# Performance work log

Measured on AMD Instinct MI355X. Metric: run time of the kernel, lower is better.

Reference implementation:

```python
import jax, jax.numpy as jnp
import numpy as np

EPS = 1e-5
N_HEAD = 16


def layernorm(x, g, b):
    mu = jnp.mean(x, axis=-1, keepdims=True)
    var = jnp.mean(jnp.square(x - mu), axis=-1, keepdims=True)
    return (x - mu) * jax.lax.rsqrt(var + EPS) * g + b


def setup_inputs() -> dict:
    key = jax.random.key(0)
    ks = jax.random.split(key, 8)
    B, S, D = 4, 2048, 1024
    F = 4 * D
    s = 0.02
    return {
        "h": jax.random.normal(ks[0], (B, S, D), jnp.float32),
        "ln1_g": jnp.ones((D,), jnp.float32),
        "ln1_b": jnp.zeros((D,), jnp.float32),
        "wq": jax.random.normal(ks[1], (D, D), jnp.float32) * s,
        "bq": jnp.zeros((D,), jnp.float32),
        "wk": jax.random.normal(ks[2], (D, D), jnp.float32) * s,
        "bk": jnp.zeros((D,), jnp.float32),
        "wv": jax.random.normal(ks[3], (D, D), jnp.float32) * s,
        "bv": jnp.zeros((D,), jnp.float32),
        "wo": jax.random.normal(ks[4], (D, D), jnp.float32) * s,
        "bo": jnp.zeros((D,), jnp.float32),
        "ln2_g": jnp.ones((D,), jnp.float32),
        "ln2_b": jnp.zeros((D,), jnp.float32),
        "wfc": jax.random.normal(ks[5], (F, D), jnp.float32) * s,
        "bfc": jnp.zeros((F,), jnp.float32),
        "wproj": jax.random.normal(ks[6], (D, F), jnp.float32) * s,
        "bproj": jnp.zeros((D,), jnp.float32),
    }


def reference(h, ln1_g, ln1_b, wq, bq, wk, bk, wv, bv, wo, bo,
              ln2_g, ln2_b, wfc, bfc, wproj, bproj):
    B, S, D = h.shape
    H = N_HEAD
    Dh = D // H

    # --- attention sub-block ---
    r = h
    x = layernorm(h, ln1_g, ln1_b)
    q = (x @ wq.T + bq).reshape(B, S, H, Dh)
    k = (x @ wk.T + bk).reshape(B, S, H, Dh)
    v = (x @ wv.T + bv).reshape(B, S, H, Dh)

    scores = jnp.einsum("bqhd,bkhd->bhqk", q, k) / jnp.sqrt(jnp.float32(Dh))
    causal = jnp.tril(jnp.ones((S, S), bool))  # [S,S]
    scores = jnp.where(causal, scores, jnp.finfo(scores.dtype).min)
    probs = jax.nn.softmax(scores, axis=-1)
    o = jnp.einsum("bhqk,bkhd->bqhd", probs, v).reshape(B, S, D)
    h = r + (o @ wo.T + bo)

    # --- MLP sub-block ---
    r = h
    x = layernorm(h, ln2_g, ln2_b)
    x = jax.nn.gelu(x @ wfc.T + bfc, approximate=True)  # NewGELU (tanh)
    h = r + (x @ wproj.T + bproj)
    return h
```

## Files before the change

### kernel.cpp

```cpp
#include <hip/hip_runtime.h>
#include <hip/hip_bf16.h>
#include <stdint.h>


typedef short bf16x8 __attribute__((ext_vector_type(8)));
typedef float f32x4  __attribute__((ext_vector_type(4)));
typedef float f32x16 __attribute__((ext_vector_type(16)));
typedef short s16x4  __attribute__((ext_vector_type(4)));

__device__ __forceinline__ short f2bf(float f) {
  union { float f; uint32_t u; } a;
  a.f = f;
  uint32_t r = a.u + 0x7fffu + ((a.u >> 16) & 1u);
  return (short)(r >> 16);
}

__device__ __forceinline__ unsigned cvt_pk_bf16(float lo, float hi_) {
  unsigned r;
  asm("v_cvt_pk_bf16_f32 %0, %1, %2" : "=v"(r) : "v"(lo), "v"(hi_));
  return r;
}

__device__ __forceinline__ float ex2(float x) {
  float r;
  asm("v_exp_f32 %0, %1" : "=v"(r) : "v"(x));
  return r;
}

__device__ __forceinline__ float rcp(float x) {
  float r;
  asm("v_rcp_f32 %0, %1" : "=v"(r) : "v"(x));
  return r;
}

__device__ __forceinline__ float m3(float a, float b, float c) {
  return fmaxf(fmaxf(a, b), c);
}

__device__ __forceinline__ void gload_lds16(const void* g, void* l) {
  __builtin_amdgcn_global_load_lds(
      (const __attribute__((address_space(1))) void*)g,
      (__attribute__((address_space(3))) void*)l, 16, 0, 0);
}

__device__ __forceinline__ float gelu_f(float x) {
  float y = 0.7978845608028654f * (x + 0.044715f * x * x * x);
  y = fminf(fmaxf(y, -20.f), 20.f);
  float e = __expf(2.f * y);
  return 0.5f * x * (1.f + (e - 1.f) / (e + 1.f));
}

struct W6 {
  const float* s[6];
  short* d[6];
  int off[7];
};

__global__ __launch_bounds__(256)
void cvt_all(W6 a) {
  const int i = blockIdx.x * 256 + threadIdx.x;
#pragma unroll
  for (int k = 0; k < 6; ++k) {
    if (i >= a.off[k] && i < a.off[k + 1]) {
      const int j = i - a.off[k];
      float4 v = ((const float4*)a.s[k])[j];
      s16x4 o;
      o[0] = f2bf(v.x); o[1] = f2bf(v.y); o[2] = f2bf(v.z); o[3] = f2bf(v.w);
      ((s16x4*)a.d[k])[j] = o;
    }
  }
}

__global__ __launch_bounds__(256)
void ln_fwd(const float* __restrict__ x, const float* __restrict__ g,
            const float* __restrict__ b, short* __restrict__ y) {
  const long row = blockIdx.x;
  const int t = threadIdx.x;
  const float4 xv = ((const float4*)(x + row * 1024))[t];
  float s  = xv.x + xv.y + xv.z + xv.w;
  float ss = xv.x * xv.x + xv.y * xv.y + xv.z * xv.z + xv.w * xv.w;
#pragma unroll
  for (int m = 1; m < 64; m <<= 1) {
    s  += __shfl_xor(s, m);
    ss += __shfl_xor(ss, m);
  }
  __shared__ float rs[4], rss[4];
  const int wid = t >> 6, lane = t & 63;
  if (lane == 0) { rs[wid] = s; rss[wid] = ss; }
  __syncthreads();
  s  = rs[0] + rs[1] + rs[2] + rs[3];
  ss = rss[0] + rss[1] + rss[2] + rss[3];
  const float mu   = s * (1.f / 1024.f);
  const float var  = ss * (1.f / 1024.f) - mu * mu;
  const float rstd = rsqrtf(var + 1e-5f);
  const float4 gv = ((const float4*)g)[t];
  const float4 bv = ((const float4*)b)[t];
  s16x4 ov;
  ov[0] = f2bf((xv.x - mu) * rstd * gv.x + bv.x);
  ov[1] = f2bf((xv.y - mu) * rstd * gv.y + bv.y);
  ov[2] = f2bf((xv.z - mu) * rstd * gv.z + bv.z);
  ov[3] = f2bf((xv.w - mu) * rstd * gv.w + bv.w);
  *(s16x4*)(y + row * 1024 + t * 4) = ov;
}

template <int OUT_BF16, int HAS_RES, int HAS_GELU, int SCALE_Q, int V_TRANS>
__global__ __launch_bounds__(256, 2)
void gemm_bt5(const short* __restrict__ A, const short* __restrict__ W,
              const float* __restrict__ bias, const float* __restrict__ res,
              void* __restrict__ out, int M, int N, int K,
              short* __restrict__ vtg, int Sp, int Hp) {
  __shared__ short As[128 * 64];
  __shared__ short Bs[256 * 64];
  const int tid = threadIdx.x;
  const int wid = tid >> 6, lane = tid & 63;
  const int l16 = lane & 15, lg = lane >> 4;
  const int wm = wid >> 1, wn = wid & 1;

  const int nbx = N >> 8;
  const int nwg = nbx * (M >> 7);
  int flat = (int)blockIdx.x;
  if ((nwg & 7) == 0) flat = (flat & 7) * (nwg >> 3) + (flat >> 3);
  const int brow = (flat / nbx) * 128, bcol = (flat % nbx) * 256;

  f32x4 acc[4][8] = {};

  const int r0 = tid >> 3, g0 = tid & 7;

  int ra[4], rb[8];
#pragma unroll
  for (int m = 0; m < 4; ++m) ra[m] = wm * 64 + m * 16 + l16;
#pragma unroll
  for (int n = 0; n < 8; ++n) rb[n] = wn * 128 + n * 16 + l16;

  for (int kt = 0; kt < K; kt += 64) {
    __syncthreads();
#pragma unroll
    for (int i = 0; i < 4; ++i) {
      const int row = i * 32 + r0;
      gload_lds16(A + (long)(brow + row) * K + kt + 8 * (g0 ^ (row & 7)),
                  &As[(i * 256 + tid) * 8]);
    }
#pragma unroll
    for (int i = 0; i < 8; ++i) {
      const int row = i * 32 + r0;
      gload_lds16(W + (long)(bcol + row) * K + kt + 8 * (g0 ^ (row & 7)),
                  &Bs[(i * 256 + tid) * 8]);
    }
    __syncthreads();

#pragma unroll
    for (int kk = 0; kk < 2; ++kk) {
      bf16x8 af[4], bf[8];
#pragma unroll
      for (int m = 0; m < 4; ++m)
        af[m] = *(const bf16x8*)&As[ra[m] * 64 + 8 * ((kk * 4 + lg) ^ (ra[m] & 7))];
#pragma unroll
      for (int n = 0; n < 8; ++n)
        bf[n] = *(const bf16x8*)&Bs[rb[n] * 64 + 8 * ((kk * 4 + lg) ^ (rb[n] & 7))];
#pragma unroll
      for (int m = 0; m < 4; ++m)
#pragma unroll
        for (int n = 0; n < 8; ++n)
          acc[m][n] = __builtin_amdgcn_mfma_f32_16x16x32_bf16(af[m], bf[n], acc[m][n], 0, 0, 0);
    }
  }

  if (V_TRANS && bcol >= 2 * (N / 3)) {
    const int bidx = brow / Sp;
    const int s0 = brow - bidx * Sp + wm * 64;
#pragma unroll
    for (int n = 0; n < 8; ++n) {
      const int col = bcol + wn * 128 + n * 16 + l16;
      const int c1 = col - 2 * (N / 3);
      const int hh = c1 >> 6, dh = c1 & 63;
      const float bb = bias[col];
      short* dst = vtg + ((long)(bidx * Hp + hh) * 64 + dh) * Sp + s0;
#pragma unroll
      for (int m = 0; m < 4; ++m) {
        s16x4 ov;
#pragma unroll
        for (int j = 0; j < 4; ++j) ov[j] = f2bf(acc[m][n][j] + bb);
        *(s16x4*)(dst + m * 16 + lg * 4) = ov;
      }
    }
    return;
  }

#pragma unroll
  for (int n = 0; n < 8; ++n) {
    const int col = bcol + wn * 128 + n * 16 + l16;
    const float bb = bias[col];
    const bool doScale = SCALE_Q && (col < N / 3);
#pragma unroll
    for (int m = 0; m < 4; ++m) {
#pragma unroll
      for (int j = 0; j < 4; ++j) {
        const long row = brow + wm * 64 + m * 16 + lg * 4 + j;
        float vv = acc[m][n][j] + bb;
        if (HAS_GELU) vv = gelu_f(vv);
        if (HAS_RES) vv += res[row * N + col];
        if (SCALE_Q && doScale) vv *= 0.18033688f;
        if (OUT_BF16) ((short*)out)[row * N + col] = f2bf(vv);
        else          ((float*)out)[row * N + col] = vv;
      }
    }
  }
}

template <int OUT_BF16, int HAS_RES, int HAS_GELU>
__global__ __launch_bounds__(256, 2)
void gemm_bt6(const short* __restrict__ A, const short* __restrict__ W,
              const float* __restrict__ bias, const float* __restrict__ res,
              void* __restrict__ out, int M, int N, int K) {
  __shared__ short As[128 * 64];
  __shared__ short Bs[128 * 64];
  const int tid = threadIdx.x;
  const int wid = tid >> 6, lane = tid & 63;
  const int l16 = lane & 15, lg = lane >> 4;
  const int wm = wid >> 1, wn = wid & 1;

  const int nbx = N >> 7;
  const int nwg = nbx * (M >> 7);
  int flat = (int)blockIdx.x;
  if ((nwg & 7) == 0) flat = (flat & 7) * (nwg >> 3) + (flat >> 3);
  const int brow = (flat / nbx) * 128, bcol = (flat % nbx) * 128;

  f32x4 acc[4][4] = {};

  const int r0 = tid >> 3, g0 = tid & 7;

  int ra[4], rb[4];
#pragma unroll
  for (int m = 0; m < 4; ++m) ra[m] = wm * 64 + m * 16 + l16;
#pragma unroll
  for (int n = 0; n < 4; ++n) rb[n] = wn * 64 + n * 16 + l16;

  for (int kt = 0; kt < K; kt += 64) {
    __syncthreads();
#pragma unroll
    for (int i = 0; i < 4; ++i) {
      const int row = i * 32 + r0;
      gload_lds16(A + (long)(brow + row) * K + kt + 8 * (g0 ^ (row & 7)),
                  &As[(i * 256 + tid) * 8]);
      gload_lds16(W + (long)(bcol + row) * K + kt + 8 * (g0 ^ (row & 7)),
                  &Bs[(i * 256 + tid) * 8]);
    }
    __syncthreads();

#pragma unroll
    for (int kk = 0; kk < 2; ++kk) {
      bf16x8 af[4], bf[4];
#pragma unroll
      for (int m = 0; m < 4; ++m)
        af[m] = *(const bf16x8*)&As[ra[m] * 64 + 8 * ((kk * 4 + lg) ^ (ra[m] & 7))];
#pragma unroll
      for (int n = 0; n < 4; ++n)
        bf[n] = *(const bf16x8*)&Bs[rb[n] * 64 + 8 * ((kk * 4 + lg) ^ (rb[n] & 7))];
#pragma unroll
      for (int m = 0; m < 4; ++m)
#pragma unroll
        for (int n = 0; n < 4; ++n)
          acc[m][n] = __builtin_amdgcn_mfma_f32_16x16x32_bf16(af[m], bf[n], acc[m][n], 0, 0, 0);
    }
  }

#pragma unroll
  for (int n = 0; n < 4; ++n) {
    const int col = bcol + wn * 64 + n * 16 + l16;
    const float bb = bias[col];
#pragma unroll
    for (int m = 0; m < 4; ++m) {
#pragma unroll
      for (int j = 0; j < 4; ++j) {
        const long row = brow + wm * 64 + m * 16 + lg * 4 + j;
        float vv = acc[m][n][j] + bb;
        if (HAS_GELU) vv = gelu_f(vv);
        if (HAS_RES) vv += res[row * N + col];
        if (OUT_BF16) ((short*)out)[row * N + col] = f2bf(vv);
        else          ((float*)out)[row * N + col] = vv;
      }
    }
  }
}

__global__ __launch_bounds__(256, 4)
void attn_fwd2(const short* __restrict__ qg, const short* __restrict__ kg,
               const short* __restrict__ vtg, short* __restrict__ og,
               int S, int ldq, int D, int H) {
  const int tid = threadIdx.x, wid = tid >> 6, lane = tid & 63;
  const int l31 = lane & 31, hi = lane >> 5;
  const int fid = blockIdx.x;
  const int bh = fid & 63;
  const int b = bh / H, hh = bh % H;
  static const int perm[16] = {15, 0, 8, 7, 1, 14, 6, 9, 13, 2, 10, 5, 3, 12, 4, 11};
  const int qt = perm[(fid >> 6) & 15];
  const int q0 = qt * 128;
  const long qbase = (long)b * S * ldq + hh * 64;
  const long obase = (long)b * S * D + hh * 64;
  const long vbase = (long)bh * 64 * S;

  __shared__ short Ks[2][64 * 64];
  __shared__ short Vs[2][64 * 64];

  auto STAGE = [&](int buf, int k0) {
#pragma unroll
    for (int i = 0; i < 2; ++i) {
      const int c = i * 256 + tid;
      const int row = c >> 3, gl = c & 7;
      gload_lds16(&kg[qbase + (long)(k0 + row) * ldq + 8 * (gl ^ (row & 7))],
                  &Ks[buf][(i * 256 + wid * 64) * 8]);
      gload_lds16(&vtg[vbase + (long)row * S + k0 + 8 * (gl ^ (row & 7))],
                  &Vs[buf][(i * 256 + wid * 64) * 8]);
    }
  };

  const int qw = q0 + wid * 32;
  const int qv = qw + l31;

  bf16x8 qf[4];
#pragma unroll
  for (int s = 0; s < 4; ++s)
    qf[s] = *(const bf16x8*)&qg[qbase + (long)qv * ldq + 16 * s + 8 * hi];

  f32x16 oa[2] = {};
  float mr = -3000.f, lr = 0.f;

  const int ntiles = qt * 2 + 2;

  STAGE(0, 0);
  for (int t = 0; t < ntiles; ++t) {
    const int cur = t & 1;
    const int k0 = t * 64;
    if (t + 1 < ntiles) {
      STAGE(cur ^ 1, k0 + 64);
      asm volatile("s_waitcnt vmcnt(4)" ::: "memory");
    } else {
      asm volatile("s_waitcnt vmcnt(0)" ::: "memory");
    }
    __builtin_amdgcn_s_barrier();

    if (k0 < qw + 32) {
      f32x16 st[2] = {};
#pragma unroll
      for (int s = 0; s < 4; ++s) {
        const int g = ((s << 1) | hi) ^ (l31 & 7);
        bf16x8 kf0 = *(const bf16x8*)&Ks[cur][l31 * 64 + 8 * g];
        bf16x8 kf1 = *(const bf16x8*)&Ks[cur][(32 + l31) * 64 + 8 * g];
        st[0] = __builtin_amdgcn_mfma_f32_32x32x16_bf16(kf0, qf[s], st[0], 0, 0, 0);
        st[1] = __builtin_amdgcn_mfma_f32_32x32x16_bf16(kf1, qf[s], st[1], 0, 0, 0);
      }

      const bool need_mask = (k0 + 63 > qw);
      float pv[2][16];
#pragma unroll
      for (int kb = 0; kb < 2; ++kb)
#pragma unroll
        for (int r = 0; r < 16; ++r) {
          float v = st[kb][r];
          if (need_mask) {
            const int key = k0 + kb * 32 + (r & 3) + 8 * (r >> 2) + 4 * hi;
            if (key > qv) v = -1e30f;
          }
          pv[kb][r] = v;
        }

      float rm = fmaxf(pv[0][0], pv[0][1]);
#pragma unroll
      for (int r = 2; r < 16; r += 2) rm = m3(rm, pv[0][r], pv[0][r + 1]);
#pragma unroll
      for (int r = 0; r < 16; r += 2) rm = m3(rm, pv[1][r], pv[1][r + 1]);
      rm = fmaxf(rm, __shfl_xor(rm, 32));

      const bool defer = (bool)__all(rm <= mr + 8.f);
      const float mn = defer ? mr : fmaxf(mr, rm);

      float a0 = 0.f, a1 = 0.f, a2 = 0.f, a3 = 0.f;
#pragma unroll
      for (int r = 0; r < 8; ++r) {
        float p0 = ex2(pv[0][r] - mn);      pv[0][r] = p0;      a0 += p0;
        float p1 = ex2(pv[0][8 + r] - mn);  pv[0][8 + r] = p1;  a1 += p1;
        float p2 = ex2(pv[1][r] - mn);      pv[1][r] = p2;      a2 += p2;
        float p3 = ex2(pv[1][8 + r] - mn);  pv[1][8 + r] = p3;  a3 += p3;
      }
      float ls = (a0 + a1) + (a2 + a3);
      ls += __shfl_xor(ls, 32);

      if (!defer) {
        const float alpha = ex2(mr - mn);
        lr = lr * alpha + ls;
        mr = mn;
#pragma unroll
        for (int r = 0; r < 16; ++r) {
          const int crow = (r & 3) + 8 * (r >> 2) + 4 * hi;
          const float ar = __shfl(alpha, crow | (lane & 32));
          oa[0][r] *= ar;
          oa[1][r] *= ar;
        }
      } else {
        lr += ls;
      }

      bf16x8 pa[4];
#pragma unroll
      for (int kb = 0; kb < 2; ++kb) {
        unsigned pk[8], ex[8];
#pragma unroll
        for (int i2 = 0; i2 < 8; ++i2)
          pk[i2] = cvt_pk_bf16(pv[kb][2 * i2], pv[kb][2 * i2 + 1]);
#pragma unroll
        for (int i2 = 0; i2 < 8; ++i2)
          ex[i2] = (unsigned)__shfl_xor((int)pk[i2], 32);
        union { unsigned u[4]; bf16x8 v8; } f0, f1;
        f0.u[0] = hi ? ex[2] : pk[0];
        f0.u[1] = hi ? ex[3] : pk[1];
        f0.u[2] = hi ? pk[2] : ex[0];
        f0.u[3] = hi ? pk[3] : ex[1];
        f1.u[0] = hi ? ex[6] : pk[4];
        f1.u[1] = hi ? ex[7] : pk[5];
        f1.u[2] = hi ? pk[6] : ex[4];
        f1.u[3] = hi ? pk[7] : ex[5];
        pa[2 * kb]     = f0.v8;
        pa[2 * kb + 1] = f1.v8;
      }

#pragma unroll
      for (int s = 0; s < 4; ++s) {
        const int g = ((s << 1) | hi) ^ (l31 & 7);
        bf16x8 vf0 = *(const bf16x8*)&Vs[cur][l31 * 64 + 8 * g];
        bf16x8 vf1 = *(const bf16x8*)&Vs[cur][(32 + l31) * 64 + 8 * g];
        oa[0] = __builtin_amdgcn_mfma_f32_32x32x16_bf16(pa[s], vf0, oa[0], 0, 0, 0);
        oa[1] = __builtin_amdgcn_mfma_f32_32x32x16_bf16(pa[s], vf1, oa[1], 0, 0, 0);
      }
    }

    asm volatile("s_waitcnt lgkmcnt(0)" ::: "memory");
    __builtin_amdgcn_s_barrier();
  }

  const float linv = rcp(lr);
#pragma unroll
  for (int r = 0; r < 16; ++r) {
    const int crow = (r & 3) + 8 * (r >> 2) + 4 * hi;
    const float li = __shfl(linv, crow | (lane & 32));
    const long row = qw + crow;
    og[obase + row * D + l31]      = f2bf(oa[0][r] * li);
    og[obase + row * D + 32 + l31] = f2bf(oa[1][r] * li);
  }
}

extern "C" void kernel_launch(void* const* d_in, const int* in_sizes, int n_in,
                              void* d_out, int out_size, void* d_ws, size_t ws_size,
                              hipStream_t stream) {
  (void)in_sizes; (void)n_in; (void)out_size; (void)ws_size;
  const float* h     = (const float*)d_in[0];
  const float* ln1_g = (const float*)d_in[1];
  const float* ln1_b = (const float*)d_in[2];
  const float* wq    = (const float*)d_in[3];
  const float* bq    = (const float*)d_in[4];
  const float* wk    = (const float*)d_in[5];
  const float* bk    = (const float*)d_in[6];
  const float* wv    = (const float*)d_in[7];
  const float* bv    = (const float*)d_in[8];
  const float* wo    = (const float*)d_in[9];
  const float* bo    = (const float*)d_in[10];
  const float* ln2_g = (const float*)d_in[11];
  const float* ln2_b = (const float*)d_in[12];
  const float* wfc   = (const float*)d_in[13];
  const float* bfc   = (const float*)d_in[14];
  const float* wproj = (const float*)d_in[15];
  const float* bproj = (const float*)d_in[16];

  const int B = 4, S = 2048, D = 1024, H = 16, F = 4096, T = B * S;
  const int D3 = 3 * D;

  char* ws = (char*)d_ws;
  size_t off = 0;
  auto alloc = [&](size_t bytes) {
    void* p = ws + off;
    off += (bytes + 255) & ~(size_t)255;
    return p;
  };
  short* xb   = (short*)alloc((size_t)T * D * 2);
  short* qkv  = (short*)alloc((size_t)T * D3 * 2);
  short* ob   = (short*)alloc((size_t)T * D * 2);
  float* h2   = (float*)alloc((size_t)T * D * 4);
  short* wqkvb  = (short*)alloc((size_t)D3 * D * 2);
  short* wob    = (short*)alloc((size_t)D * D * 2);
  short* wfcb   = (short*)alloc((size_t)F * D * 2);
  short* wprojb = (short*)alloc((size_t)D * F * 2);
  float* bqkv   = (float*)alloc((size_t)D3 * 4);
  short* ub  = qkv;
  short* vtg = (short*)h2;

  W6 wargs;
  const int nqq = D * D / 4;
  wargs.s[0] = wq;    wargs.d[0] = wqkvb;
  wargs.s[1] = wk;    wargs.d[1] = wqkvb + (size_t)D * D;
  wargs.s[2] = wv;    wargs.d[2] = wqkvb + (size_t)2 * D * D;
  wargs.s[3] = wo;    wargs.d[3] = wob;
  wargs.s[4] = wfc;   wargs.d[4] = wfcb;
  wargs.s[5] = wproj; wargs.d[5] = wprojb;
  wargs.off[0] = 0;
  wargs.off[1] = nqq;
  wargs.off[2] = 2 * nqq;
  wargs.off[3] = 3 * nqq;
  wargs.off[4] = 4 * nqq;
  wargs.off[5] = 4 * nqq + F * D / 4;
  wargs.off[6] = 4 * nqq + 2 * (F * D / 4);
  cvt_all<<<dim3(wargs.off[6] / 256), 256, 0, stream>>>(wargs);
  hipMemcpyAsync(bqkv,         bq, D * 4, hipMemcpyDeviceToDevice, stream);
  hipMemcpyAsync(bqkv + D,     bk, D * 4, hipMemcpyDeviceToDevice, stream);
  hipMemcpyAsync(bqkv + 2 * D, bv, D * 4, hipMemcpyDeviceToDevice, stream);

  ln_fwd<<<dim3(T), 256, 0, stream>>>(h, ln1_g, ln1_b, xb);
  gemm_bt5<1, 0, 0, 1, 1><<<dim3((T / 128) * (D3 / 256)), 256, 0, stream>>>(
      xb, wqkvb, bqkv, nullptr, qkv, T, D3, D, vtg, S, H);
  attn_fwd2<<<dim3((S / 128) * (B * H / 64) * 64), 256, 0, stream>>>(
      qkv, qkv + D, vtg, ob, S, D3, D, H);
  gemm_bt6<0, 1, 0><<<dim3((T / 128) * (D / 128)), 256, 0, stream>>>(
      ob, wob, bo, h, h2, T, D, D);

  ln_fwd<<<dim3(T), 256, 0, stream>>>(h2, ln2_g, ln2_b, xb);
  gemm_bt5<1, 0, 1, 0, 0><<<dim3((T / 128) * (F / 256)), 256, 0, stream>>>(
      xb, wfcb, bfc, nullptr, ub, T, F, D, nullptr, 0, 0);
  gemm_bt6<0, 1, 0><<<dim3((T / 128) * (D / 128)), 256, 0, stream>>>(
      ub, wprojb, bproj, h2, (float*)d_out, T, D, F);
}
```

Measured before the change: 368.7 us.

## Split long causal attention query tiles across two blocks with merge kernel

Query tiles 8-15 now have their key range split into two halves, each processed by a separate block. The partial outputs (stored as bf16) and the row max and row sum go to a workspace, and a new merge kernel combines them with the usual log-sum-exp rescaling. A fixed 24-entry schedule orders the work so the heaviest pieces start first. The goal is to balance load across CUs and remove the long tail from the causal triangle. The cost is an extra kernel launch, extra workspace traffic, and a bf16 rounding of the unnormalised partial outputs.

```diff
diff --git a/kernel.cpp b/kernel.cpp
--- a/kernel.cpp
+++ b/kernel.cpp
@@ -13,6 +13,12 @@
   a.f = f;
   uint32_t r = a.u + 0x7fffu + ((a.u >> 16) & 1u);
   return (short)(r >> 16);
+}
+
+__device__ __forceinline__ float bf2f(short s) {
+  union { uint32_t u; float f; } x;
+  x.u = ((uint32_t)(unsigned short)s) << 16;
+  return x.f;
 }
 
 __device__ __forceinline__ unsigned cvt_pk_bf16(float lo, float hi_) {
@@ -286,14 +292,26 @@
 __global__ __launch_bounds__(256, 4)
 void attn_fwd2(const short* __restrict__ qg, const short* __restrict__ kg,
                const short* __restrict__ vtg, short* __restrict__ og,
+               short* __restrict__ pO, float* __restrict__ pm,
+               float* __restrict__ pl,
                int S, int ldq, int D, int H) {
   const int tid = threadIdx.x, wid = tid >> 6, lane = tid & 63;
   const int l31 = lane & 31, hi = lane >> 5;
   const int fid = blockIdx.x;
+  static const int sched[24] = {
+      7, 47, 63, 46, 62, 6, 45, 61, 44, 60, 5, 43,
+      59, 42, 58, 4, 41, 57, 40, 56, 3, 2, 1, 0};
+  const int cls = sched[fid >> 6];
   const int bh = fid & 63;
+  const int qt = cls & 15;
+  const int part = (cls >> 4) & 1;
+  const bool split = (cls & 32) != 0;
+  const int nt = qt * 2 + 2;
+  const int hl = nt >> 1;
+  const int t0 = split ? (part ? hl : 0) : 0;
+  const int t1 = split ? (part ? nt : hl) : nt;
+
   const int b = bh / H, hh = bh % H;
-  static const int perm[16] = {15, 0, 8, 7, 1, 14, 6, 9, 13, 2, 10, 5, 3, 12, 4, 11};
-  const int qt = perm[(fid >> 6) & 15];
   const int q0 = qt * 128;
   const long qbase = (long)b * S * ldq + hh * 64;
   const long obase = (long)b * S * D + hh * 64;
@@ -325,13 +343,11 @@
   f32x16 oa[2] = {};
   float mr = -3000.f, lr = 0.f;
 
-  const int ntiles = qt * 2 + 2;
-
-  STAGE(0, 0);
-  for (int t = 0; t < ntiles; ++t) {
-    const int cur = t & 1;
+  STAGE(0, t0 * 64);
+  for (int t = t0; t < t1; ++t) {
+    const int cur = (t - t0) & 1;
     const int k0 = t * 64;
-    if (t + 1 < ntiles) {
+    if (t + 1 < t1) {
       STAGE(cur ^ 1, k0 + 64);
       asm volatile("s_waitcnt vmcnt(4)" ::: "memory");
     } else {
@@ -437,14 +453,60 @@
     __builtin_amdgcn_s_barrier();
   }
 
-  const float linv = rcp(lr);
-#pragma unroll
-  for (int r = 0; r < 16; ++r) {
-    const int crow = (r & 3) + 8 * (r >> 2) + 4 * hi;
-    const float li = __shfl(linv, crow | (lane & 32));
-    const long row = qw + crow;
-    og[obase + row * D + l31]      = f2bf(oa[0][r] * li);
-    og[obase + row * D + 32 + l31] = f2bf(oa[1][r] * li);
+  if (!split) {
+    const float linv = rcp(lr);
+#pragma unroll
+    for (int r = 0; r < 16; ++r) {
+      const int crow = (r & 3) + 8 * (r >> 2) + 4 * hi;
+      const float li = __shfl(linv, crow | (lane & 32));
+      const long row = qw + crow;
+      og[obase + row * D + l31]      = f2bf(oa[0][r] * li);
+      og[obase + row * D + 32 + l31] = f2bf(oa[1][r] * li);
+    }
+  } else {
+    const int pabs = part * 512 + (((qt - 8) << 6) | bh);
+    short* dst = pO + (long)pabs * 128 * 64;
+    if (hi == 0) {
+      pm[pabs * 128 + wid * 32 + l31] = mr;
+      pl[pabs * 128 + wid * 32 + l31] = lr;
+    }
+#pragma unroll
+    for (int r = 0; r < 16; ++r) {
+      const int crow = (r & 3) + 8 * (r >> 2) + 4 * hi;
+      const int row = wid * 32 + crow;
+      dst[row * 64 + l31]      = f2bf(oa[0][r]);
+      dst[row * 64 + 32 + l31] = f2bf(oa[1][r]);
+    }
+  }
+}
+
+__global__ __launch_bounds__(256)
+void attn_merge(const short* __restrict__ pO, const float* __restrict__ pm,
+                const float* __restrict__ pl, short* __restrict__ og,
+                int S, int D, int H) {
+  const int pslot = blockIdx.x;
+  const int qt = 8 + (pslot >> 6), bh = pslot & 63;
+  const int b = bh / H, hh = bh % H;
+  const int t = threadIdx.x;
+  const int r = t >> 1, ch = (t & 1) << 5;
+  const float m1 = pm[pslot * 128 + r], m2 = pm[(512 + pslot) * 128 + r];
+  const float l1 = pl[pslot * 128 + r], l2 = pl[(512 + pslot) * 128 + r];
+  const float mm = fmaxf(m1, m2);
+  const float w1 = ex2(m1 - mm), w2 = ex2(m2 - mm);
+  const float li = rcp(l1 * w1 + l2 * w2);
+  const float f1 = w1 * li, f2 = w2 * li;
+  const short* s1 = pO + ((long)pslot * 128 + r) * 64 + ch;
+  const short* s2 = pO + ((long)(512 + pslot) * 128 + r) * 64 + ch;
+  short* d = og + (long)(b * S + qt * 128 + r) * D + hh * 64 + ch;
+#pragma unroll
+  for (int i = 0; i < 4; ++i) {
+    bf16x8 a = *(const bf16x8*)(s1 + i * 8);
+    bf16x8 c = *(const bf16x8*)(s2 + i * 8);
+    bf16x8 ov;
+#pragma unroll
+    for (int j = 0; j < 8; ++j)
+      ov[j] = f2bf(bf2f(a[j]) * f1 + bf2f(c[j]) * f2);
+    *(bf16x8*)(d + i * 8) = ov;
   }
 }
 
@@ -489,6 +551,9 @@
   short* wfcb   = (short*)alloc((size_t)F * D * 2);
   short* wprojb = (short*)alloc((size_t)D * F * 2);
   float* bqkv   = (float*)alloc((size_t)D3 * 4);
+  short* pO  = (short*)alloc((size_t)1024 * 128 * 64 * 2);
+  float* pmb = (float*)alloc((size_t)1024 * 128 * 4);
+  float* plb = (float*)alloc((size_t)1024 * 128 * 4);
   short* ub  = qkv;
   short* vtg = (short*)h2;
 
@@ -515,8 +580,9 @@
   ln_fwd<<<dim3(T), 256, 0, stream>>>(h, ln1_g, ln1_b, xb);
   gemm_bt5<1, 0, 0, 1, 1><<<dim3((T / 128) * (D3 / 256)), 256, 0, stream>>>(
       xb, wqkvb, bqkv, nullptr, qkv, T, D3, D, vtg, S, H);
-  attn_fwd2<<<dim3((S / 128) * (B * H / 64) * 64), 256, 0, stream>>>(
-      qkv, qkv + D, vtg, ob, S, D3, D, H);
+  attn_fwd2<<<dim3(24 * 64), 256, 0, stream>>>(
+      qkv, qkv + D, vtg, ob, pO, pmb, plb, S, D3, D, H);
+  attn_merge<<<dim3(512), 256, 0, stream>>>(pO, pmb, plb, ob, S, D, H);
   gemm_bt6<0, 1, 0><<<dim3((T / 128) * (D / 128)), 256, 0, stream>>>(
       ob, wob, bo, h, h2, T, D, D);
 
```

Measured after the change: 368.9 us. Within noise of the previous version (+0.1%).
